# Kernel optimization log

Measured on AMD Instinct MI355X. Metric: run time of the kernel, lower is better.

The kernel has to match this reference:

```python
import jax, jax.numpy as jnp
import numpy as np

B, N, C, H = 4, 2048, 1024, 16
D = C // H  # head_dim = 64
SCALE = D ** -0.5


def setup_inputs() -> dict:
    key = jax.random.key(0)
    ks = jax.random.split(key, 7)
    # freqs_cis = exp(i*theta): unit-modulus rotations, as in standard RoPE
    theta = jax.random.uniform(ks[1], (B, N, D // 2), jnp.float32, 0.0, 2 * np.pi)
    return {
        "x": jax.random.normal(ks[0], (B, N, C), jnp.float32),
        "freqs_cos": jnp.cos(theta),
        "freqs_sin": jnp.sin(theta),
        "attn_mask": jax.random.normal(ks[2], (1, 1, N, N), jnp.float32) * 0.1,
        "Wqkv": jax.random.normal(ks[3], (3 * C, C), jnp.float32) * (C ** -0.5),
        "Wproj": jax.random.normal(ks[4], (C, C), jnp.float32) * (C ** -0.5),
        "bproj": jnp.zeros((C,), jnp.float32),
    }


def _rope(t, cos, sin):
    # t: [B,H,N,D]; cos/sin: [B,1,N,D/2]; complex multiply on interleaved pairs
    tr = t.reshape(*t.shape[:-1], D // 2, 2)
    t0, t1 = tr[..., 0], tr[..., 1]
    out = jnp.stack([t0 * cos - t1 * sin, t0 * sin + t1 * cos], axis=-1)
    return out.reshape(t.shape)


def reference(x, freqs_cos, freqs_sin, attn_mask, Wqkv, Wproj, bproj):
    qkv = x @ Wqkv.T  # [B,N,3C]
    qkv = qkv.reshape(B, N, 3, H, D).transpose(2, 0, 3, 1, 4)  # [3,B,H,N,D]
    q, k, v = qkv[0], qkv[1], qkv[2]
    cos = freqs_cos[:, None]  # [B,1,N,D/2]
    sin = freqs_sin[:, None]
    q = _rope(q, cos, sin)
    k = _rope(k, cos, sin)
    attn = jnp.einsum("bhnd,bhmd->bhnm", q * SCALE, k) + attn_mask
    attn = jax.nn.softmax(attn, axis=-1)
    out = jnp.einsum("bhnm,bhmd->bhnd", attn, v)  # [B,H,N,D]
    out = out.transpose(0, 2, 1, 3).reshape(B, N, C)
    return out @ Wproj.T + bproj
```

## Files before the change

kernel.cpp:

```cpp
#include <hip/hip_runtime.h>
#include <hip/hip_bf16.h>
#include <stdint.h>


typedef __bf16 bf16;
typedef __bf16 bf16x4 __attribute__((ext_vector_type(4)));
typedef __bf16 bf16x8 __attribute__((ext_vector_type(8)));
typedef float  f32x4  __attribute__((ext_vector_type(4)));
typedef float  f32x16 __attribute__((ext_vector_type(16)));
typedef int    int4v  __attribute__((ext_vector_type(4)));

#define MFMA16(a, b, c) __builtin_amdgcn_mfma_f32_16x16x32_bf16((a), (b), (c), 0, 0, 0)
#define MFMA32(a, b, c) __builtin_amdgcn_mfma_f32_32x32x16_bf16((a), (b), (c), 0, 0, 0)

__device__ __forceinline__ bf16x4 cvt4s(float a, float b, float c, float d) {
  bf16x4 r;
  r[0] = (bf16)a; r[1] = (bf16)b; r[2] = (bf16)c; r[3] = (bf16)d;
  return r;
}
__device__ __forceinline__ bf16x8 cvt8(f32x4 a, f32x4 b) {
  bf16x8 r;
  r[0] = (bf16)a[0]; r[1] = (bf16)a[1]; r[2] = (bf16)a[2]; r[3] = (bf16)a[3];
  r[4] = (bf16)b[0]; r[5] = (bf16)b[1]; r[6] = (bf16)b[2]; r[7] = (bf16)b[3];
  return r;
}

template<int MODE>
__global__ __launch_bounds__(256)
void gemm_bt(const void* __restrict__ Av, const float* __restrict__ B,
             void* __restrict__ O0, bf16* __restrict__ O1, bf16* __restrict__ O2,
             const float* __restrict__ bias)
{
  constexpr int K = 1024;
  __shared__ __attribute__((aligned(16))) bf16 As[128 * 64];
  __shared__ __attribute__((aligned(16))) bf16 Bs[128 * 64];
  const int tid = threadIdx.x, lane = tid & 63, wid = tid >> 6;
  const int m0 = blockIdx.x * 128, n0 = blockIdx.y * 128;
  const int wm = (wid >> 1) * 64, wn = (wid & 1) * 64;
  const int l15 = lane & 15, lg = lane >> 4;

  f32x4 acc[4][4] = {};

  for (int k0 = 0; k0 < K; k0 += 64) {
#pragma unroll
    for (int it = 0; it < 4; ++it) {
      const int e = (it * 256 + tid) * 8;
      const int row = e >> 6, col = e & 63;
      const float* bp = B + (size_t)(n0 + row) * K + k0 + col;
      *(bf16x8*)(Bs + row * 64 + col) =
          cvt8(*(const f32x4*)bp, *(const f32x4*)(bp + 4));
    }
    if (MODE == 0) {
      const float* A = (const float*)Av;
#pragma unroll
      for (int it = 0; it < 4; ++it) {
        const int e = (it * 256 + tid) * 8;
        const int row = e >> 6, col = e & 63;
        const float* ap = A + (size_t)(m0 + row) * K + k0 + col;
        *(bf16x8*)(As + row * 64 + col) =
            cvt8(*(const f32x4*)ap, *(const f32x4*)(ap + 4));
      }
    } else {
      const bf16* A = (const bf16*)Av;
#pragma unroll
      for (int it = 0; it < 4; ++it) {
        const int e = (it * 256 + tid) * 8;
        const int row = e >> 6, col = e & 63;
        *(bf16x8*)(As + row * 64 + col) =
            *(const bf16x8*)(A + (size_t)(m0 + row) * K + k0 + col);
      }
    }
    __syncthreads();

    bf16x8 af[4][2], bb[4][2];
#pragma unroll
    for (int i = 0; i < 4; ++i)
#pragma unroll
      for (int kk = 0; kk < 2; ++kk) {
        af[i][kk] = *(const bf16x8*)(As + (wm + i * 16 + l15) * 64 + kk * 32 + lg * 8);
        bb[i][kk] = *(const bf16x8*)(Bs + (wn + i * 16 + l15) * 64 + kk * 32 + lg * 8);
      }
#pragma unroll
    for (int mi = 0; mi < 4; ++mi)
#pragma unroll
      for (int ni = 0; ni < 4; ++ni)
#pragma unroll
        for (int kk = 0; kk < 2; ++kk)
          acc[mi][ni] = MFMA16(af[mi][kk], bb[ni][kk], acc[mi][ni]);
    __syncthreads();
  }

#pragma unroll
  for (int mi = 0; mi < 4; ++mi)
#pragma unroll
    for (int ni = 0; ni < 4; ++ni)
#pragma unroll
      for (int r = 0; r < 4; ++r) {
        const int row = m0 + wm + mi * 16 + lg * 4 + r;
        const int col = n0 + wn + ni * 16 + l15;
        float v = acc[mi][ni][r];
        if (MODE == 0) {
          const int s = col >> 10, h = (col >> 6) & 15, d = col & 63;
          const int b = row >> 11, n = row & 2047;
          const bf16 bv = (bf16)v;
          if (s == 0)
            ((bf16*)O0)[(((size_t)(b * 16 + h) * 2048) + n) * 64 + d] = bv;
          else if (s == 1)
            O1[(((size_t)(b * 16 + h) * 2048) + n) * 64 + d] = bv;
          else
            O2[(((size_t)(b * 16 + h) * 64) + d) * 2048 + n] = bv;
        } else {
          ((float*)O0)[(size_t)row * 1024 + col] = v + bias[col];
        }
      }
}

__global__ __launch_bounds__(256)
void rope_k(bf16* __restrict__ Q, bf16* __restrict__ K,
            const float* __restrict__ C, const float* __restrict__ S)
{
  const int gid = blockIdx.x * 256 + threadIdx.x;
  const int part = gid & 3;
  const int rowid = gid >> 2;
  const int n = rowid & 2047;
  const int b = rowid >> 15;
  const size_t cbase = ((size_t)(b * 2048 + n)) * 32 + part * 8;

  float cf[8], sf[8];
  *(f32x4*)cf = *(const f32x4*)(C + cbase);
  *(f32x4*)(cf + 4) = *(const f32x4*)(C + cbase + 4);
  *(f32x4*)sf = *(const f32x4*)(S + cbase);
  *(f32x4*)(sf + 4) = *(const f32x4*)(S + cbase + 4);

  bf16* qp = Q + (size_t)rowid * 64 + part * 16;
  bf16* kp = K + (size_t)rowid * 64 + part * 16;
  __attribute__((aligned(16))) bf16 buf[16];

  *(int4v*)buf = *(const int4v*)qp;
  *(int4v*)(buf + 8) = *(const int4v*)(qp + 8);
#pragma unroll
  for (int j = 0; j < 8; ++j) {
    const float t0 = (float)buf[2 * j], t1 = (float)buf[2 * j + 1];
    buf[2 * j]     = (bf16)(t0 * cf[j] - t1 * sf[j]);
    buf[2 * j + 1] = (bf16)(t0 * sf[j] + t1 * cf[j]);
  }
  *(int4v*)qp = *(int4v*)buf;
  *(int4v*)(qp + 8) = *(int4v*)(buf + 8);

  *(int4v*)buf = *(const int4v*)kp;
  *(int4v*)(buf + 8) = *(const int4v*)(kp + 8);
#pragma unroll
  for (int j = 0; j < 8; ++j) {
    const float t0 = (float)buf[2 * j], t1 = (float)buf[2 * j + 1];
    buf[2 * j]     = (bf16)(t0 * cf[j] - t1 * sf[j]);
    buf[2 * j + 1] = (bf16)(t0 * sf[j] + t1 * cf[j]);
  }
  *(int4v*)kp = *(int4v*)buf;
  *(int4v*)(kp + 8) = *(int4v*)(buf + 8);
}

__global__ __launch_bounds__(256, 4)
void attn_k(const bf16* __restrict__ Q, const bf16* __restrict__ K,
            const bf16* __restrict__ VT, const float* __restrict__ M,
             bf16* __restrict__ O)
{
  constexpr float SCALE_LOG2E = 0.125f * 1.4426950408889634f;
  constexpr float LOG2E = 1.4426950408889634f;
  __shared__ __attribute__((aligned(16))) bf16 SH[9216];
  bf16* Kt = SH;
  bf16* Vt = SH + 4096;

  const int tid = threadIdx.x, lane = tid & 63, w = tid >> 6;
  const int bh = blockIdx.x;
  const int q0 = blockIdx.y * 128;
  const int b = bh >> 4, h = bh & 15;
  const int l31 = lane & 31, hi = lane >> 5;
  const int swz = (l31 & 7) << 3;

  const bf16* Qb = Q + (size_t)bh * 2048 * 64;
  const bf16* Kb = K + (size_t)bh * 2048 * 64;
  const bf16* Vb = VT + (size_t)bh * 64 * 2048;
  const float* Mq = M + (size_t)(q0 + w * 32 + l31) * 2048;

  bf16x8 qf[4];
  {
    const bf16* qr = Qb + (size_t)(q0 + w * 32 + l31) * 64 + 8 * hi;
#pragma unroll
    for (int j = 0; j < 4; ++j) qf[j] = *(const bf16x8*)(qr + 16 * j);
  }

  f32x16 o[2] = {{0,0,0,0,0,0,0,0,0,0,0,0,0,0,0,0},
                 {0,0,0,0,0,0,0,0,0,0,0,0,0,0,0,0}};
  float li = 0.f;

  for (int kv0 = 0; kv0 < 2048; kv0 += 64) {
#pragma unroll
    for (int it = 0; it < 2; ++it) {
      const int idx = it * 256 + tid;
      const int row = idx >> 3, g8 = (idx & 7) * 8;
      const int sc = g8 ^ ((row & 7) << 3);
      *(int4v*)(Kt + row * 64 + sc) =
          *(const int4v*)(Kb + (size_t)(kv0 + row) * 64 + g8);
      *(int4v*)(Vt + row * 64 + sc) =
          *(const int4v*)(Vb + (size_t)row * 2048 + kv0 + g8);
    }

    f32x4 mk_all[2][4];
#pragma unroll
    for (int sub = 0; sub < 2; ++sub)
#pragma unroll
      for (int rg = 0; rg < 4; ++rg)
        mk_all[sub][rg] = *(const f32x4*)(Mq + kv0 + 32 * sub + 8 * rg + 4 * hi);

    __syncthreads();

#pragma unroll
    for (int sub = 0; sub < 2; ++sub) {
      f32x16 s = {0,0,0,0,0,0,0,0,0,0,0,0,0,0,0,0};
#pragma unroll
      for (int j = 0; j < 4; ++j) {
        const bf16x8 kf = *(const bf16x8*)(
            Kt + (sub * 32 + l31) * 64 + ((16 * j + 8 * hi) ^ swz));
        s = MFMA32(kf, qf[j], s);
      }

      float rs = 0.f;
#pragma unroll
      for (int rg = 0; rg < 4; ++rg)
#pragma unroll
        for (int i = 0; i < 4; ++i) {
          const float p = __builtin_exp2f(
              fmaf(s[4 * rg + i], SCALE_LOG2E, mk_all[sub][rg][i] * LOG2E));
          s[4 * rg + i] = p;
          rs += p;
        }
      rs += __shfl_xor(rs, 32);
      li += rs;

      uint32_t pk0, pk1, pk2, pk3, pk4, pk5, pk6, pk7;
      asm("v_cvt_pk_bf16_f32 %0, %1, %2" : "=v"(pk0) : "v"(s[0]),  "v"(s[1]));
      asm("v_cvt_pk_bf16_f32 %0, %1, %2" : "=v"(pk1) : "v"(s[2]),  "v"(s[3]));
      asm("v_cvt_pk_bf16_f32 %0, %1, %2" : "=v"(pk2) : "v"(s[4]),  "v"(s[5]));
      asm("v_cvt_pk_bf16_f32 %0, %1, %2" : "=v"(pk3) : "v"(s[6]),  "v"(s[7]));
      asm("v_cvt_pk_bf16_f32 %0, %1, %2" : "=v"(pk4) : "v"(s[8]),  "v"(s[9]));
      asm("v_cvt_pk_bf16_f32 %0, %1, %2" : "=v"(pk5) : "v"(s[10]), "v"(s[11]));
      asm("v_cvt_pk_bf16_f32 %0, %1, %2" : "=v"(pk6) : "v"(s[12]), "v"(s[13]));
      asm("v_cvt_pk_bf16_f32 %0, %1, %2" : "=v"(pk7) : "v"(s[14]), "v"(s[15]));
      asm("v_permlane32_swap_b32 %0, %1" : "+v"(pk0), "+v"(pk2));
      asm("v_permlane32_swap_b32 %0, %1" : "+v"(pk1), "+v"(pk3));
      asm("v_permlane32_swap_b32 %0, %1" : "+v"(pk4), "+v"(pk6));
      asm("v_permlane32_swap_b32 %0, %1" : "+v"(pk5), "+v"(pk7));
      uint32_t pau[2][4] = {{pk0, pk1, pk2, pk3}, {pk4, pk5, pk6, pk7}};
      bf16x8 pa[2];
      __builtin_memcpy(&pa[0], pau[0], 16);
      __builtin_memcpy(&pa[1], pau[1], 16);

#pragma unroll
      for (int kh = 0; kh < 2; ++kh)
#pragma unroll
        for (int dblk = 0; dblk < 2; ++dblk) {
          const bf16x8 vf = *(const bf16x8*)(
              Vt + (dblk * 32 + l31) * 64 + ((sub * 32 + kh * 16 + 8 * hi) ^ swz));
          o[dblk] = MFMA32(vf, pa[kh], o[dblk]);
        }
    }
    __syncthreads();
  }

  const float inv = 1.f / li;
  bf16* ow = SH + w * 2304;
#pragma unroll
  for (int dblk = 0; dblk < 2; ++dblk)
#pragma unroll
    for (int rg = 0; rg < 4; ++rg)
      *(bf16x4*)(ow + l31 * 72 + dblk * 32 + 8 * rg + 4 * hi) =
          cvt4s(o[dblk][4 * rg] * inv, o[dblk][4 * rg + 1] * inv,
                o[dblk][4 * rg + 2] * inv, o[dblk][4 * rg + 3] * inv);
  asm volatile("s_waitcnt lgkmcnt(0)" ::: "memory");
  __builtin_amdgcn_sched_barrier(0);
#pragma unroll
  for (int p = 0; p < 4; ++p) {
    const int row = p * 8 + (lane >> 3);
    const int n = q0 + w * 32 + row;
    const int4v v = *(const int4v*)(ow + row * 72 + (lane & 7) * 8);
    *(int4v*)(O + ((size_t)b * 2048 + n) * 1024 + h * 64 + (lane & 7) * 8) = v;
  }
}

extern "C" void kernel_launch(void* const* d_in, const int* in_sizes, int n_in,
                              void* d_out, int out_size, void* d_ws, size_t ws_size,
                              hipStream_t stream)
{
  (void)in_sizes; (void)n_in; (void)out_size;
  const float* x     = (const float*)d_in[0];
  const float* fcos  = (const float*)d_in[1];
  const float* fsin  = (const float*)d_in[2];
  const float* mask  = (const float*)d_in[3];
  const float* wqkv  = (const float*)d_in[4];
  const float* wproj = (const float*)d_in[5];
  const float* bproj = (const float*)d_in[6];
  float* out = (float*)d_out;

  const size_t SZ = (size_t)64 * 2048 * 64 * 2;
  if (ws_size < 4 * SZ) return;
  char* ws = (char*)d_ws;
  bf16* Qr = (bf16*)(ws);
  bf16* Kr = (bf16*)(ws + SZ);
  bf16* VT = (bf16*)(ws + 2 * SZ);
  bf16* Ob = (bf16*)(ws + 3 * SZ);

  gemm_bt<0><<<dim3(64, 24), 256, 0, stream>>>(x, wqkv, Qr, Kr, VT, nullptr);
  rope_k<<<2048, 256, 0, stream>>>(Qr, Kr, fcos, fsin);
  attn_k<<<dim3(64, 16), 256, 0, stream>>>(Qr, Kr, VT, mask, Ob);
  gemm_bt<1><<<dim3(64, 8), 256, 0, stream>>>(Ob, wproj, out, nullptr, nullptr, bproj);
}
```

Baseline: 320.7 us.

## Pre-convert weights to bf16, use LDS direct loads, split attention KV across groups

```diff
diff --git a/kernel.cpp b/kernel.cpp
--- a/kernel.cpp
+++ b/kernel.cpp
@@ -24,10 +24,22 @@
   r[4] = (bf16)b[0]; r[5] = (bf16)b[1]; r[6] = (bf16)b[2]; r[7] = (bf16)b[3];
   return r;
 }
+__device__ __forceinline__ void gload16(const void* g, void* l) {
+  __builtin_amdgcn_global_load_lds((const __attribute__((address_space(1))) void*)g,
+                                   (__attribute__((address_space(3))) void*)l, 16, 0, 0);
+}
+
+__global__ __launch_bounds__(256)
+void cvt_k(const float* __restrict__ W, bf16* __restrict__ Wb)
+{
+  const size_t i = ((size_t)blockIdx.x * 256 + threadIdx.x) * 8;
+  const float* p = W + i;
+  *(bf16x8*)(Wb + i) = cvt8(*(const f32x4*)p, *(const f32x4*)(p + 4));
+}
 
 template<int MODE>
 __global__ __launch_bounds__(256)
-void gemm_bt(const void* __restrict__ Av, const float* __restrict__ B,
+void gemm_bt(const void* __restrict__ Av, const bf16* __restrict__ B,
              void* __restrict__ O0, bf16* __restrict__ O1, bf16* __restrict__ O2,
              const float* __restrict__ bias)
 {
@@ -43,12 +55,12 @@
 
   for (int k0 = 0; k0 < K; k0 += 64) {
 #pragma unroll
-    for (int it = 0; it < 4; ++it) {
-      const int e = (it * 256 + tid) * 8;
-      const int row = e >> 6, col = e & 63;
-      const float* bp = B + (size_t)(n0 + row) * K + k0 + col;
-      *(bf16x8*)(Bs + row * 64 + col) =
-          cvt8(*(const f32x4*)bp, *(const f32x4*)(bp + 4));
+    for (int c = 0; c < 4; ++c) {
+      const int seg = wid * 4 + c;
+      const int o = seg * 1024 + lane * 16;
+      const int row = o >> 7, colb = o & 127;
+      gload16((const char*)B + (((size_t)(n0 + row) * K + k0) << 1) + colb,
+              (char*)Bs + seg * 1024);
     }
     if (MODE == 0) {
       const float* A = (const float*)Av;
@@ -63,11 +75,12 @@
     } else {
       const bf16* A = (const bf16*)Av;
 #pragma unroll
-      for (int it = 0; it < 4; ++it) {
-        const int e = (it * 256 + tid) * 8;
-        const int row = e >> 6, col = e & 63;
-        *(bf16x8*)(As + row * 64 + col) =
-            *(const bf16x8*)(A + (size_t)(m0 + row) * K + k0 + col);
+      for (int c = 0; c < 4; ++c) {
+        const int seg = wid * 4 + c;
+        const int o = seg * 1024 + lane * 16;
+        const int row = o >> 7, colb = o & 127;
+        gload16((const char*)A + (((size_t)(m0 + row) * K + k0) << 1) + colb,
+                (char*)As + seg * 1024);
       }
     }
     __syncthreads();
@@ -159,32 +172,34 @@
   *(int4v*)(kp + 8) = *(int4v*)(buf + 8);
 }
 
-__global__ __launch_bounds__(256, 4)
+__global__ __launch_bounds__(512, 8)
 void attn_k(const bf16* __restrict__ Q, const bf16* __restrict__ K,
             const bf16* __restrict__ VT, const float* __restrict__ M,
-             bf16* __restrict__ O)
+            bf16* __restrict__ O)
 {
   constexpr float SCALE_LOG2E = 0.125f * 1.4426950408889634f;
   constexpr float LOG2E = 1.4426950408889634f;
-  __shared__ __attribute__((aligned(16))) bf16 SH[9216];
-  bf16* Kt = SH;
-  bf16* Vt = SH + 4096;
+  __shared__ __attribute__((aligned(16))) bf16 SH[16896];
 
   const int tid = threadIdx.x, lane = tid & 63, w = tid >> 6;
+  const int g = w >> 2, wg = w & 3, tg = tid & 255;
   const int bh = blockIdx.x;
   const int q0 = blockIdx.y * 128;
   const int b = bh >> 4, h = bh & 15;
   const int l31 = lane & 31, hi = lane >> 5;
   const int swz = (l31 & 7) << 3;
 
+  bf16* Kt = SH + g * 8192;
+  bf16* Vt = Kt + 4096;
+
   const bf16* Qb = Q + (size_t)bh * 2048 * 64;
-  const bf16* Kb = K + (size_t)bh * 2048 * 64;
-  const bf16* Vb = VT + (size_t)bh * 64 * 2048;
-  const float* Mq = M + (size_t)(q0 + w * 32 + l31) * 2048;
+  const bf16* Kb = K + (size_t)bh * 2048 * 64 + (size_t)g * 1024 * 64;
+  const bf16* Vb = VT + (size_t)bh * 64 * 2048 + g * 1024;
+  const float* Mq = M + (size_t)(q0 + wg * 32 + l31) * 2048 + g * 1024;
 
   bf16x8 qf[4];
   {
-    const bf16* qr = Qb + (size_t)(q0 + w * 32 + l31) * 64 + 8 * hi;
+    const bf16* qr = Qb + (size_t)(q0 + wg * 32 + l31) * 64 + 8 * hi;
 #pragma unroll
     for (int j = 0; j < 4; ++j) qf[j] = *(const bf16x8*)(qr + 16 * j);
   }
@@ -193,10 +208,10 @@
                  {0,0,0,0,0,0,0,0,0,0,0,0,0,0,0,0}};
   float li = 0.f;
 
-  for (int kv0 = 0; kv0 < 2048; kv0 += 64) {
+  for (int kv0 = 0; kv0 < 1024; kv0 += 64) {
 #pragma unroll
     for (int it = 0; it < 2; ++it) {
-      const int idx = it * 256 + tid;
+      const int idx = it * 256 + tg;
       const int row = idx >> 3, g8 = (idx & 7) * 8;
       const int sc = g8 ^ ((row & 7) << 3);
       *(int4v*)(Kt + row * 64 + sc) =
@@ -204,7 +219,6 @@
       *(int4v*)(Vt + row * 64 + sc) =
           *(const int4v*)(Vb + (size_t)row * 2048 + kv0 + g8);
     }
-
     f32x4 mk_all[2][4];
 #pragma unroll
     for (int sub = 0; sub < 2; ++sub)
@@ -267,8 +281,41 @@
     __syncthreads();
   }
 
-  const float inv = 1.f / li;
-  bf16* ow = SH + w * 2304;
+  float* CB = (float*)SH;
+  if (g == 1) {
+    if (hi == 0) CB[8192 + wg * 32 + l31] = li;
+    float* cb = CB + wg * 2048;
+#pragma unroll
+    for (int dblk = 0; dblk < 2; ++dblk)
+#pragma unroll
+      for (int rg = 0; rg < 4; ++rg) {
+        const int dbase = dblk * 32 + 8 * rg + 4 * hi;
+        const int off = dbase ^ ((l31 & 15) << 2);
+        *(f32x4*)(cb + l31 * 64 + off) =
+            (f32x4){o[dblk][4 * rg], o[dblk][4 * rg + 1],
+                    o[dblk][4 * rg + 2], o[dblk][4 * rg + 3]};
+      }
+  }
+  __syncthreads();
+  float inv = 0.f;
+  if (g == 0) {
+    const float li_tot = li + CB[8192 + wg * 32 + l31];
+    float* cb = CB + wg * 2048;
+#pragma unroll
+    for (int dblk = 0; dblk < 2; ++dblk)
+#pragma unroll
+      for (int rg = 0; rg < 4; ++rg) {
+        const int dbase = dblk * 32 + 8 * rg + 4 * hi;
+        const f32x4 part = *(const f32x4*)(cb + l31 * 64 + (dbase ^ ((l31 & 15) << 2)));
+#pragma unroll
+        for (int i = 0; i < 4; ++i) o[dblk][4 * rg + i] += part[i];
+      }
+    inv = 1.f / li_tot;
+  }
+  __syncthreads();
+  if (g == 1) return;
+
+  bf16* ow = SH + wg * 2304;
 #pragma unroll
   for (int dblk = 0; dblk < 2; ++dblk)
 #pragma unroll
@@ -281,7 +328,7 @@
 #pragma unroll
   for (int p = 0; p < 4; ++p) {
     const int row = p * 8 + (lane >> 3);
-    const int n = q0 + w * 32 + row;
+    const int n = q0 + wg * 32 + row;
     const int4v v = *(const int4v*)(ow + row * 72 + (lane & 7) * 8);
     *(int4v*)(O + ((size_t)b * 2048 + n) * 1024 + h * 64 + (lane & 7) * 8) = v;
   }
@@ -302,15 +349,21 @@
   float* out = (float*)d_out;
 
   const size_t SZ = (size_t)64 * 2048 * 64 * 2;
-  if (ws_size < 4 * SZ) return;
+  const size_t WQB = (size_t)3072 * 1024 * 2;
+  const size_t WPB = (size_t)1024 * 1024 * 2;
+  if (ws_size < 4 * SZ + WQB + WPB) return;
   char* ws = (char*)d_ws;
-  bf16* Qr = (bf16*)(ws);
-  bf16* Kr = (bf16*)(ws + SZ);
-  bf16* VT = (bf16*)(ws + 2 * SZ);
-  bf16* Ob = (bf16*)(ws + 3 * SZ);
-
-  gemm_bt<0><<<dim3(64, 24), 256, 0, stream>>>(x, wqkv, Qr, Kr, VT, nullptr);
+  bf16* Qr  = (bf16*)(ws);
+  bf16* Kr  = (bf16*)(ws + SZ);
+  bf16* VT  = (bf16*)(ws + 2 * SZ);
+  bf16* Ob  = (bf16*)(ws + 3 * SZ);
+  bf16* Wqb = (bf16*)(ws + 4 * SZ);
+  bf16* Wpb = (bf16*)(ws + 4 * SZ + WQB);
+
+  cvt_k<<<1536, 256, 0, stream>>>(wqkv, Wqb);
+  cvt_k<<<512, 256, 0, stream>>>(wproj, Wpb);
+  gemm_bt<0><<<dim3(64, 24), 256, 0, stream>>>(x, Wqb, Qr, Kr, VT, nullptr);
   rope_k<<<2048, 256, 0, stream>>>(Qr, Kr, fcos, fsin);
-  attn_k<<<dim3(64, 16), 256, 0, stream>>>(Qr, Kr, VT, mask, Ob);
-  gemm_bt<1><<<dim3(64, 8), 256, 0, stream>>>(Ob, wproj, out, nullptr, nullptr, bproj);
-}
+  attn_k<<<dim3(64, 16), 512, 0, stream>>>(Qr, Kr, VT, mask, Ob);
+  gemm_bt<1><<<dim3(64, 8), 256, 0, stream>>>(Ob, Wpb, out, nullptr, nullptr, bproj);
+}
```

Result: slower. 1.034 ms (+222.4%).
